# Performance work log

Hardware: AMD Instinct MI355X
Metric: run time of the kernel (lower is better)

The kernel has to match this reference:

```python
import jax, jax.numpy as jnp
import numpy as np


def _sample_plane(plane, coords):
    """torch.nn.functional.grid_sample, mode='bilinear', padding_mode='zeros',
    align_corners=True.  plane: [C,H,W]; coords: [N,2] with (x,y) in [-1,1]
    (x indexes W, y indexes H, as in torch grid convention).  Returns [N,C]."""
    C, H, W = plane.shape
    x = (coords[:, 0] + 1.0) * 0.5 * (W - 1)
    y = (coords[:, 1] + 1.0) * 0.5 * (H - 1)
    x0f = jnp.floor(x); y0f = jnp.floor(y)
    wx = x - x0f; wy = y - y0f

    def corner(yi, xi):
        valid = (xi >= 0) & (xi < W) & (yi >= 0) & (yi < H)
        xc = jnp.clip(xi, 0, W - 1).astype(jnp.int32)
        yc = jnp.clip(yi, 0, H - 1).astype(jnp.int32)
        return plane[:, yc, xc] * valid.astype(plane.dtype)  # [C,N]

    v00 = corner(y0f, x0f)
    v01 = corner(y0f, x0f + 1)
    v10 = corner(y0f + 1, x0f)
    v11 = corner(y0f + 1, x0f + 1)
    out = (v00 * (1 - wx) * (1 - wy) + v01 * wx * (1 - wy)
           + v10 * (1 - wx) * wy + v11 * wx * wy)
    return out.T  # [N,C]


_sample_batched = jax.vmap(_sample_plane)  # [B,C,H,W],[B,N,2] -> [B,N,C]


def setup_inputs() -> dict:
    key = jax.random.key(0)
    ks = jax.random.split(key, 8)
    B, N, C, R = 4, 131072, 32, 256
    triplanes = jax.random.normal(ks[0], (B, 3, C, R, R), jnp.float32) * 0.1
    coordinates = jax.random.uniform(ks[1], (B, N, 3), jnp.float32, -1.0, 1.0)
    # MLP weights ~ frequency_init(30) / first_layer_sine_init scales
    w0 = jax.random.uniform(ks[2], (128, C), jnp.float32, -1.0 / C, 1.0 / C)
    b0 = jnp.zeros((128,), jnp.float32)
    s1 = np.sqrt(6.0 / 128) / 30.0
    w1 = jax.random.uniform(ks[3], (128, 128), jnp.float32, -s1, s1)
    b1 = jnp.zeros((128,), jnp.float32)
    w2 = jax.random.uniform(ks[4], (1, 128), jnp.float32, -s1, s1)
    b2 = jnp.zeros((1,), jnp.float32)
    return {"triplanes": triplanes, "coordinates": coordinates,
            "w0": w0, "b0": b0, "w1": w1, "b1": b1, "w2": w2, "b2": b2}


def reference(triplanes, coordinates, w0, b0, w1, b1, w2, b2):
    # triplanes: [B,3,C,R,R]; coordinates: [B,N,3]
    xy = _sample_batched(triplanes[:, 0], coordinates[..., 0:2])   # (x,y)
    yz = _sample_batched(triplanes[:, 1], coordinates[..., 1:3])   # (y,z)
    xz = _sample_batched(triplanes[:, 2], coordinates[..., 0::2])  # (x,z)
    features = xy * yz * xz  # aggregate_fn == 'prod'; [B,N,C]
    h = jax.nn.relu(jnp.einsum('bnc,hc->bnh', features, w0) + b0)
    h = jax.nn.relu(jnp.einsum('bnh,gh->bng', h, w1) + b1)
    return jnp.einsum('bng,og->bno', h, w2) + b2  # [B,N,1]
```

## Files before the change

kernel.cpp:

```cpp
#include <hip/hip_runtime.h>
#include <hip/hip_bf16.h>
#include <cstddef>

#define RES 256
#define NCH 32
#define NPT 131072
#define NB  4

typedef _Float16 half8 __attribute__((ext_vector_type(8)));
typedef _Float16 half4 __attribute__((ext_vector_type(4)));
typedef float    f32x4 __attribute__((ext_vector_type(4)));

#define H0_STRIDE 136

__global__ __launch_bounds__(256) void transpose_fp16_kernel(
    const float* __restrict__ in, _Float16* __restrict__ out)
{
    __shared__ _Float16 tileh[NCH][2 * RES];
    const int bp = blockIdx.y;
    const int y2 = blockIdx.x;
    const int t  = threadIdx.x;

    const float4* src4 = (const float4*)(in + (size_t)bp * NCH * RES * RES);
    const int f4l = t & 127;
    const int chalf = t >> 7;
    #pragma unroll
    for (int i = 0; i < 16; ++i) {
        const int c = i * 2 + chalf;
        const float4 v = src4[(size_t)c * (RES * RES / 4) + y2 * 128 + f4l];
        half4 h = { (_Float16)v.x, (_Float16)v.y, (_Float16)v.z, (_Float16)v.w };
        *(half4*)&tileh[c][f4l * 4] = h;
    }
    __syncthreads();

    _Float16* dst = out + ((size_t)bp * RES * RES + (size_t)y2 * 512) * NCH;
    #pragma unroll
    for (int rep = 0; rep < 2; ++rep) {
        const int x = rep * 256 + t;
        #pragma unroll
        for (int cg = 0; cg < 4; ++cg) {
            half8 h;
            #pragma unroll
            for (int k = 0; k < 8; ++k)
                h[k] = tileh[cg * 8 + k][x];
            *(half8*)&dst[(size_t)x * NCH + cg * 8] = h;
        }
    }
}

__global__ __launch_bounds__(256) void prep_weights(
    const float* __restrict__ w0, const float* __restrict__ w1,
    _Float16* __restrict__ w0h, _Float16* __restrict__ w1h)
{
    const int i = blockIdx.x * 256 + threadIdx.x;
    if (i < 128 * NCH) w0h[i] = (_Float16)(w0[i] * 16.0f);
    if (i < 128 * 128) w1h[i] = (_Float16)w1[i];
}

__global__ __launch_bounds__(256, 4) void sample_kernel(
    const _Float16* __restrict__ planesT,
    const float* __restrict__ coords,
    _Float16* __restrict__ featOut)
{
    const int gid = blockIdx.x * 256 + threadIdx.x;
    const int pt  = gid >> 1;
    const int hf  = gid & 1;
    const int b   = pt >> 17;

    const float cx = coords[(size_t)pt * 3 + 0];
    const float cy = coords[(size_t)pt * 3 + 1];
    const float cz = coords[(size_t)pt * 3 + 2];

    float f[3][16];
    #pragma unroll
    for (int pl = 0; pl < 3; ++pl) {
        const float u = (pl == 0) ? cx : (pl == 1) ? cy : cx;
        const float v = (pl == 0) ? cy : cz;

        const float fx = (u + 1.0f) * 0.5f * (RES - 1);
        const float fy = (v + 1.0f) * 0.5f * (RES - 1);
        const float x0f = floorf(fx), y0f = floorf(fy);
        const float wx = fx - x0f, wy = fy - y0f;
        const int x0 = (int)x0f, y0 = (int)y0f;
        const bool vx1 = (x0 + 1) < RES;
        const bool vy1 = (y0 + 1) < RES;
        const int x1 = vx1 ? x0 + 1 : RES - 1;
        const int y1 = vy1 ? y0 + 1 : RES - 1;

        float w00 = (1.0f - wx) * (1.0f - wy);
        float w01 = wx * (1.0f - wy);
        float w10 = (1.0f - wx) * wy;
        float w11 = wx * wy;
        if (!vx1) { w01 = 0.0f; w11 = 0.0f; }
        if (!vy1) { w10 = 0.0f; w11 = 0.0f; }

        const _Float16* base = planesT
            + ((size_t)(b * 3 + pl) * RES * RES) * NCH + hf * 16;

        const half8* p00 = (const half8*)(base + (size_t)(y0 * RES + x0) * NCH);
        const half8* p01 = (const half8*)(base + (size_t)(y0 * RES + x1) * NCH);
        const half8* p10 = (const half8*)(base + (size_t)(y1 * RES + x0) * NCH);
        const half8* p11 = (const half8*)(base + (size_t)(y1 * RES + x1) * NCH);

        const half8 a00 = p00[0], b00 = p00[1];
        const half8 a01 = p01[0], b01 = p01[1];
        const half8 a10 = p10[0], b10 = p10[1];
        const half8 a11 = p11[0], b11 = p11[1];

        #pragma unroll
        for (int k = 0; k < 8; ++k) {
            f[pl][k] = fmaf((float)a11[k], w11, fmaf((float)a10[k], w10,
                       fmaf((float)a01[k], w01, (float)a00[k] * w00)));
            f[pl][8 + k] = fmaf((float)b11[k], w11, fmaf((float)b10[k], w10,
                           fmaf((float)b01[k], w01, (float)b00[k] * w00)));
        }
    }

    half8 o0, o1;
    #pragma unroll
    for (int k = 0; k < 8; ++k) {
        o0[k] = (_Float16)(f[0][k]     * f[1][k]     * f[2][k]     * 256.0f);
        o1[k] = (_Float16)(f[0][8 + k] * f[1][8 + k] * f[2][8 + k] * 256.0f);
    }
    _Float16* dst = featOut + (size_t)pt * NCH + hf * 16;
    *(half8*)&dst[0] = o0;
    *(half8*)&dst[8] = o1;
}

__global__ __launch_bounds__(256, 4) void gemm_kernel(
    const _Float16* __restrict__ feat,
    const _Float16* __restrict__ w0h,
    const _Float16* __restrict__ w1h,
    const float* __restrict__ b0, const float* __restrict__ b1,
    const float* __restrict__ w2, const float* __restrict__ b2,
    float* __restrict__ out)
{
    __shared__ __align__(16) _Float16 h0LDS[4][32 * H0_STRIDE];

    const int tid  = threadIdx.x;
    const int wv   = tid >> 6;
    const int lane = tid & 63;
    const int l15  = lane & 15;
    const int quad = lane >> 4;

    const int m0 = blockIdx.x * 128 + wv * 32;

    half8 a0[2];
    #pragma unroll
    for (int mt = 0; mt < 2; ++mt)
        a0[mt] = *(const half8*)&feat[(size_t)(m0 + mt * 16 + l15) * NCH + quad * 8];

    #pragma unroll 1
    for (int nt = 0; nt < 8; ++nt) {
        const half8 bfr = *(const half8*)&w0h[(nt * 16 + l15) * NCH + quad * 8];
        const float b0g = b0[nt * 16 + l15] * 4096.0f;
        f32x4 acc[2];
        #pragma unroll
        for (int mt = 0; mt < 2; ++mt) {
            acc[mt] = (f32x4){0.f, 0.f, 0.f, 0.f};
            acc[mt] = __builtin_amdgcn_mfma_f32_16x16x32_f16(
                a0[mt], bfr, acc[mt], 0, 0, 0);
        }
        #pragma unroll
        for (int mt = 0; mt < 2; ++mt)
            #pragma unroll
            for (int r = 0; r < 4; ++r) {
                const float hval = fmaxf(acc[mt][r] + b0g, 0.0f);
                h0LDS[wv][(mt * 16 + quad * 4 + r) * H0_STRIDE + nt * 16 + l15]
                    = (_Float16)hval;
            }
    }

    half8 a1[2][4];
    #pragma unroll
    for (int mt = 0; mt < 2; ++mt)
        #pragma unroll
        for (int ks = 0; ks < 4; ++ks)
            a1[mt][ks] = *(const half8*)
                &h0LDS[wv][(mt * 16 + l15) * H0_STRIDE + ks * 32 + quad * 8];

    float part[2][4];
    #pragma unroll
    for (int mt = 0; mt < 2; ++mt)
        #pragma unroll
        for (int r = 0; r < 4; ++r) part[mt][r] = 0.0f;

    #pragma unroll 1
    for (int nt = 0; nt < 8; ++nt) {
        const float b1g = b1[nt * 16 + l15] * 4096.0f;
        const float w2g = w2[nt * 16 + l15] * (1.0f / 4096.0f);
        f32x4 acc[2];
        #pragma unroll
        for (int mt = 0; mt < 2; ++mt) acc[mt] = (f32x4){0.f, 0.f, 0.f, 0.f};
        #pragma unroll
        for (int ks = 0; ks < 4; ++ks) {
            const half8 bfr = *(const half8*)
                &w1h[(nt * 16 + l15) * 128 + ks * 32 + quad * 8];
            #pragma unroll
            for (int mt = 0; mt < 2; ++mt)
                acc[mt] = __builtin_amdgcn_mfma_f32_16x16x32_f16(
                    a1[mt][ks], bfr, acc[mt], 0, 0, 0);
        }
        #pragma unroll
        for (int mt = 0; mt < 2; ++mt)
            #pragma unroll
            for (int r = 0; r < 4; ++r)
                part[mt][r] = fmaf(w2g, fmaxf(acc[mt][r] + b1g, 0.0f), part[mt][r]);
    }

    #pragma unroll
    for (int mt = 0; mt < 2; ++mt)
        #pragma unroll
        for (int r = 0; r < 4; ++r) {
            float s = part[mt][r];
            s += __shfl_xor(s, 1);
            s += __shfl_xor(s, 2);
            s += __shfl_xor(s, 4);
            s += __shfl_xor(s, 8);
            part[mt][r] = s;
        }

    if (l15 == 0) {
        const float bias2 = b2[0];
        #pragma unroll
        for (int mt = 0; mt < 2; ++mt)
            #pragma unroll
            for (int r = 0; r < 4; ++r)
                out[m0 + mt * 16 + quad * 4 + r] = part[mt][r] + bias2;
    }
}

__global__ __launch_bounds__(256) void fused_fallback(
    const float* __restrict__ planes, const float* __restrict__ coords,
    const float* __restrict__ w0, const float* __restrict__ b0,
    const float* __restrict__ w1, const float* __restrict__ b1,
    const float* __restrict__ w2, const float* __restrict__ b2,
    float* __restrict__ out)
{
    const int t = blockIdx.x * 256 + threadIdx.x;
    const int b = t >> 17;
    const float cx = coords[(size_t)t * 3 + 0];
    const float cy = coords[(size_t)t * 3 + 1];
    const float cz = coords[(size_t)t * 3 + 2];
    float feat[NCH];
    #pragma unroll
    for (int p = 0; p < 3; ++p) {
        const float u = (p == 0) ? cx : (p == 1) ? cy : cx;
        const float v = (p == 0) ? cy : cz;
        const float fx = (u + 1.0f) * 0.5f * (RES - 1);
        const float fy = (v + 1.0f) * 0.5f * (RES - 1);
        const float x0f = floorf(fx), y0f = floorf(fy);
        const float wx = fx - x0f, wy = fy - y0f;
        const int x0 = (int)x0f, y0 = (int)y0f;
        const bool vx1 = (x0 + 1) < RES, vy1 = (y0 + 1) < RES;
        const int x1 = vx1 ? x0 + 1 : RES - 1;
        const int y1 = vy1 ? y0 + 1 : RES - 1;
        float w00 = (1.0f - wx) * (1.0f - wy), w01 = wx * (1.0f - wy);
        float w10 = (1.0f - wx) * wy, w11 = wx * wy;
        if (!vx1) { w01 = 0.0f; w11 = 0.0f; }
        if (!vy1) { w10 = 0.0f; w11 = 0.0f; }
        const float* base = planes + (size_t)(b * 3 + p) * NCH * RES * RES;
        const float* p00 = base + (size_t)y0 * RES + x0;
        const float* p01 = base + (size_t)y0 * RES + x1;
        const float* p10 = base + (size_t)y1 * RES + x0;
        const float* p11 = base + (size_t)y1 * RES + x1;
        #pragma unroll
        for (int c = 0; c < NCH; ++c) {
            const size_t off = (size_t)c * RES * RES;
            float s = p00[off] * w00;
            s = fmaf(p01[off], w01, s);
            s = fmaf(p10[off], w10, s);
            s = fmaf(p11[off], w11, s);
            if (p == 0) feat[c] = s; else feat[c] *= s;
        }
    }
    float h0[128];
    #pragma unroll
    for (int g = 0; g < 128; ++g) {
        const float* wr = w0 + g * NCH;
        float aA = b0[g], aB = 0.0f;
        #pragma unroll
        for (int c = 0; c < NCH; c += 2) {
            aA = fmaf(wr[c], feat[c], aA);
            aB = fmaf(wr[c + 1], feat[c + 1], aB);
        }
        h0[g] = fmaxf(aA + aB, 0.0f);
    }
    float o = b2[0];
    for (int g = 0; g < 128; ++g) {
        const float* wr = w1 + g * 128;
        float aA = b1[g], aB = 0.0f, aC = 0.0f, aD = 0.0f;
        #pragma unroll
        for (int h = 0; h < 128; h += 4) {
            aA = fmaf(wr[h], h0[h], aA);
            aB = fmaf(wr[h + 1], h0[h + 1], aB);
            aC = fmaf(wr[h + 2], h0[h + 2], aC);
            aD = fmaf(wr[h + 3], h0[h + 3], aD);
        }
        o = fmaf(fmaxf((aA + aB) + (aC + aD), 0.0f), w2[g], o);
    }
    out[t] = o;
}

extern "C" void kernel_launch(void* const* d_in, const int* in_sizes, int n_in,
                              void* d_out, int out_size, void* d_ws, size_t ws_size,
                              hipStream_t stream)
{
    const float* trip   = (const float*)d_in[0];
    const float* coords = (const float*)d_in[1];
    const float* w0     = (const float*)d_in[2];
    const float* b0     = (const float*)d_in[3];
    const float* w1     = (const float*)d_in[4];
    const float* b1     = (const float*)d_in[5];
    const float* w2     = (const float*)d_in[6];
    const float* b2     = (const float*)d_in[7];
    float* out = (float*)d_out;

    const size_t planesTBytes = (size_t)NB * 3 * RES * RES * NCH * 2;
    const size_t w0hBytes  = 128 * NCH * 2;
    const size_t w1hBytes  = 128 * 128 * 2;
    const size_t featBytes = (size_t)NB * NPT * NCH * 2;
    const size_t needed = planesTBytes + w0hBytes + w1hBytes + featBytes;

    if (ws_size >= needed) {
        _Float16* planesT = (_Float16*)d_ws;
        _Float16* w0h     = (_Float16*)((char*)d_ws + planesTBytes);
        _Float16* w1h     = (_Float16*)((char*)d_ws + planesTBytes + w0hBytes);
        _Float16* featWS  = (_Float16*)((char*)d_ws + planesTBytes + w0hBytes + w1hBytes);

        transpose_fp16_kernel<<<dim3(RES / 2, NB * 3), 256, 0, stream>>>(trip, planesT);
        prep_weights<<<64, 256, 0, stream>>>(w0, w1, w0h, w1h);
        sample_kernel<<<(NB * NPT * 2) / 256, 256, 0, stream>>>(planesT, coords, featWS);
        gemm_kernel<<<(NB * NPT) / 128, 256, 0, stream>>>(
            featWS, w0h, w1h, b0, b1, w2, b2, out);
    } else {
        fused_fallback<<<(NB * NPT) / 256, 256, 0, stream>>>(
            trip, coords, w0, b0, w1, b1, w2, b2, out);
    }
}
```

Measured before the change: 333.4 us.

## Fuse triplane sampling into MLP kernel via shared-memory feature staging

Merges the sampling kernel and the MLP GEMM kernel into one. Each block now samples its 128 points into a padded LDS tile, which aliases the hidden-layer buffer, and then runs the MFMA layers directly on it. This removes the fp16 feature round-trip through global memory and one kernel launch. Bias and w2 values are preloaded into registers, and the transpose kernel now handles one row per block with a padded LDS tile. The trade-off is a lower occupancy hint (256,2), so fewer waves are resident to hide the gather latency.

```diff
diff --git a/kernel.cpp b/kernel.cpp
--- a/kernel.cpp
+++ b/kernel.cpp
@@ -11,40 +11,38 @@
 typedef _Float16 half4 __attribute__((ext_vector_type(4)));
 typedef float    f32x4 __attribute__((ext_vector_type(4)));
 
-#define H0_STRIDE 136
+#define FEAT_STRIDE 40
+#define H0_STRIDE   136
 
 __global__ __launch_bounds__(256) void transpose_fp16_kernel(
     const float* __restrict__ in, _Float16* __restrict__ out)
 {
-    __shared__ _Float16 tileh[NCH][2 * RES];
+    __shared__ _Float16 tileh[NCH][RES + 8];
     const int bp = blockIdx.y;
-    const int y2 = blockIdx.x;
+    const int y  = blockIdx.x;
     const int t  = threadIdx.x;
 
     const float4* src4 = (const float4*)(in + (size_t)bp * NCH * RES * RES);
-    const int f4l = t & 127;
-    const int chalf = t >> 7;
-    #pragma unroll
-    for (int i = 0; i < 16; ++i) {
-        const int c = i * 2 + chalf;
-        const float4 v = src4[(size_t)c * (RES * RES / 4) + y2 * 128 + f4l];
+    const int lane64 = t & 63;
+    const int cq     = t >> 6;
+    #pragma unroll
+    for (int i = 0; i < 8; ++i) {
+        const int c = cq * 8 + i;
+        const float4 v = src4[(size_t)c * (RES * RES / 4) + y * (RES / 4) + lane64];
         half4 h = { (_Float16)v.x, (_Float16)v.y, (_Float16)v.z, (_Float16)v.w };
-        *(half4*)&tileh[c][f4l * 4] = h;
+        *(half4*)&tileh[c][lane64 * 4] = h;
     }
     __syncthreads();
 
-    _Float16* dst = out + ((size_t)bp * RES * RES + (size_t)y2 * 512) * NCH;
-    #pragma unroll
-    for (int rep = 0; rep < 2; ++rep) {
-        const int x = rep * 256 + t;
-        #pragma unroll
-        for (int cg = 0; cg < 4; ++cg) {
-            half8 h;
-            #pragma unroll
-            for (int k = 0; k < 8; ++k)
-                h[k] = tileh[cg * 8 + k][x];
-            *(half8*)&dst[(size_t)x * NCH + cg * 8] = h;
-        }
+    _Float16* dst = out + ((size_t)bp * RES * RES + (size_t)y * RES) * NCH;
+    const int x = t;
+    #pragma unroll
+    for (int cg = 0; cg < 4; ++cg) {
+        half8 h;
+        #pragma unroll
+        for (int k = 0; k < 8; ++k)
+            h[k] = tileh[cg * 8 + k][x];
+        *(half8*)&dst[(size_t)x * NCH + cg * 8] = h;
     }
 }
 
@@ -57,85 +55,18 @@
     if (i < 128 * 128) w1h[i] = (_Float16)w1[i];
 }
 
-__global__ __launch_bounds__(256, 4) void sample_kernel(
+__global__ __launch_bounds__(256, 2) void fused_kernel(
     const _Float16* __restrict__ planesT,
     const float* __restrict__ coords,
-    _Float16* __restrict__ featOut)
-{
-    const int gid = blockIdx.x * 256 + threadIdx.x;
-    const int pt  = gid >> 1;
-    const int hf  = gid & 1;
-    const int b   = pt >> 17;
-
-    const float cx = coords[(size_t)pt * 3 + 0];
-    const float cy = coords[(size_t)pt * 3 + 1];
-    const float cz = coords[(size_t)pt * 3 + 2];
-
-    float f[3][16];
-    #pragma unroll
-    for (int pl = 0; pl < 3; ++pl) {
-        const float u = (pl == 0) ? cx : (pl == 1) ? cy : cx;
-        const float v = (pl == 0) ? cy : cz;
-
-        const float fx = (u + 1.0f) * 0.5f * (RES - 1);
-        const float fy = (v + 1.0f) * 0.5f * (RES - 1);
-        const float x0f = floorf(fx), y0f = floorf(fy);
-        const float wx = fx - x0f, wy = fy - y0f;
-        const int x0 = (int)x0f, y0 = (int)y0f;
-        const bool vx1 = (x0 + 1) < RES;
-        const bool vy1 = (y0 + 1) < RES;
-        const int x1 = vx1 ? x0 + 1 : RES - 1;
-        const int y1 = vy1 ? y0 + 1 : RES - 1;
-
-        float w00 = (1.0f - wx) * (1.0f - wy);
-        float w01 = wx * (1.0f - wy);
-        float w10 = (1.0f - wx) * wy;
-        float w11 = wx * wy;
-        if (!vx1) { w01 = 0.0f; w11 = 0.0f; }
-        if (!vy1) { w10 = 0.0f; w11 = 0.0f; }
-
-        const _Float16* base = planesT
-            + ((size_t)(b * 3 + pl) * RES * RES) * NCH + hf * 16;
-
-        const half8* p00 = (const half8*)(base + (size_t)(y0 * RES + x0) * NCH);
-        const half8* p01 = (const half8*)(base + (size_t)(y0 * RES + x1) * NCH);
-        const half8* p10 = (const half8*)(base + (size_t)(y1 * RES + x0) * NCH);
-        const half8* p11 = (const half8*)(base + (size_t)(y1 * RES + x1) * NCH);
-
-        const half8 a00 = p00[0], b00 = p00[1];
-        const half8 a01 = p01[0], b01 = p01[1];
-        const half8 a10 = p10[0], b10 = p10[1];
-        const half8 a11 = p11[0], b11 = p11[1];
-
-        #pragma unroll
-        for (int k = 0; k < 8; ++k) {
-            f[pl][k] = fmaf((float)a11[k], w11, fmaf((float)a10[k], w10,
-                       fmaf((float)a01[k], w01, (float)a00[k] * w00)));
-            f[pl][8 + k] = fmaf((float)b11[k], w11, fmaf((float)b10[k], w10,
-                           fmaf((float)b01[k], w01, (float)b00[k] * w00)));
-        }
-    }
-
-    half8 o0, o1;
-    #pragma unroll
-    for (int k = 0; k < 8; ++k) {
-        o0[k] = (_Float16)(f[0][k]     * f[1][k]     * f[2][k]     * 256.0f);
-        o1[k] = (_Float16)(f[0][8 + k] * f[1][8 + k] * f[2][8 + k] * 256.0f);
-    }
-    _Float16* dst = featOut + (size_t)pt * NCH + hf * 16;
-    *(half8*)&dst[0] = o0;
-    *(half8*)&dst[8] = o1;
-}
-
-__global__ __launch_bounds__(256, 4) void gemm_kernel(
-    const _Float16* __restrict__ feat,
     const _Float16* __restrict__ w0h,
     const _Float16* __restrict__ w1h,
     const float* __restrict__ b0, const float* __restrict__ b1,
     const float* __restrict__ w2, const float* __restrict__ b2,
     float* __restrict__ out)
 {
-    __shared__ __align__(16) _Float16 h0LDS[4][32 * H0_STRIDE];
+    __shared__ __align__(16) _Float16 smem[4 * 32 * H0_STRIDE];
+    _Float16* featLDS = smem;
+    _Float16* h0LDS   = smem;
 
     const int tid  = threadIdx.x;
     const int wv   = tid >> 6;
@@ -143,17 +74,91 @@
     const int l15  = lane & 15;
     const int quad = lane >> 4;
 
-    const int m0 = blockIdx.x * 128 + wv * 32;
+    {
+        const int p  = tid >> 1;
+        const int hf = tid & 1;
+        const int gp = blockIdx.x * 128 + p;
+        const int b  = gp >> 17;
+        const float cx = coords[(size_t)gp * 3 + 0];
+        const float cy = coords[(size_t)gp * 3 + 1];
+        const float cz = coords[(size_t)gp * 3 + 2];
+
+        float f[3][16];
+        #pragma unroll
+        for (int pl = 0; pl < 3; ++pl) {
+            const float u = (pl == 0) ? cx : (pl == 1) ? cy : cx;
+            const float v = (pl == 0) ? cy : cz;
+
+            const float fx = (u + 1.0f) * 0.5f * (RES - 1);
+            const float fy = (v + 1.0f) * 0.5f * (RES - 1);
+            const float x0f = floorf(fx), y0f = floorf(fy);
+            const float wx = fx - x0f, wy = fy - y0f;
+            const int x0 = (int)x0f, y0 = (int)y0f;
+            const bool vx1 = (x0 + 1) < RES;
+            const bool vy1 = (y0 + 1) < RES;
+            const int x1 = vx1 ? x0 + 1 : RES - 1;
+            const int y1 = vy1 ? y0 + 1 : RES - 1;
+
+            float w00 = (1.0f - wx) * (1.0f - wy);
+            float w01 = wx * (1.0f - wy);
+            float w10 = (1.0f - wx) * wy;
+            float w11 = wx * wy;
+            if (!vx1) { w01 = 0.0f; w11 = 0.0f; }
+            if (!vy1) { w10 = 0.0f; w11 = 0.0f; }
+
+            const _Float16* base = planesT
+                + ((size_t)(b * 3 + pl) * RES * RES) * NCH + hf * 16;
+
+            const half8* p00 = (const half8*)(base + (size_t)(y0 * RES + x0) * NCH);
+            const half8* p01 = (const half8*)(base + (size_t)(y0 * RES + x1) * NCH);
+            const half8* p10 = (const half8*)(base + (size_t)(y1 * RES + x0) * NCH);
+            const half8* p11 = (const half8*)(base + (size_t)(y1 * RES + x1) * NCH);
+
+            const half8 a00 = p00[0], b00 = p00[1];
+            const half8 a01 = p01[0], b01 = p01[1];
+            const half8 a10 = p10[0], b10 = p10[1];
+            const half8 a11 = p11[0], b11 = p11[1];
+
+            #pragma unroll
+            for (int k = 0; k < 8; ++k) {
+                f[pl][k] = fmaf((float)a11[k], w11, fmaf((float)a10[k], w10,
+                           fmaf((float)a01[k], w01, (float)a00[k] * w00)));
+                f[pl][8 + k] = fmaf((float)b11[k], w11, fmaf((float)b10[k], w10,
+                               fmaf((float)b01[k], w01, (float)b00[k] * w00)));
+            }
+        }
+        half8 o0, o1;
+        #pragma unroll
+        for (int k = 0; k < 8; ++k) {
+            o0[k] = (_Float16)(f[0][k]     * f[1][k]     * f[2][k]     * 256.0f);
+            o1[k] = (_Float16)(f[0][8 + k] * f[1][8 + k] * f[2][8 + k] * 256.0f);
+        }
+        *(half8*)&featLDS[p * FEAT_STRIDE + hf * 16 + 0] = o0;
+        *(half8*)&featLDS[p * FEAT_STRIDE + hf * 16 + 8] = o1;
+    }
+
+    const int m0l = wv * 32;
 
     half8 a0[2];
     #pragma unroll
     for (int mt = 0; mt < 2; ++mt)
-        a0[mt] = *(const half8*)&feat[(size_t)(m0 + mt * 16 + l15) * NCH + quad * 8];
+        a0[mt] = *(const half8*)&featLDS[(m0l + mt * 16 + l15) * FEAT_STRIDE + quad * 8];
+
+    __syncthreads();
+
+    float b0v[8], b1v[8], w2s[8];
+    #pragma unroll
+    for (int nt = 0; nt < 8; ++nt) {
+        b0v[nt] = b0[nt * 16 + l15] * 4096.0f;
+        b1v[nt] = b1[nt * 16 + l15] * 4096.0f;
+        w2s[nt] = w2[nt * 16 + l15] * (1.0f / 4096.0f);
+    }
+
+    _Float16* h0w = h0LDS + wv * 32 * H0_STRIDE;
 
     #pragma unroll 1
     for (int nt = 0; nt < 8; ++nt) {
         const half8 bfr = *(const half8*)&w0h[(nt * 16 + l15) * NCH + quad * 8];
-        const float b0g = b0[nt * 16 + l15] * 4096.0f;
         f32x4 acc[2];
         #pragma unroll
         for (int mt = 0; mt < 2; ++mt) {
@@ -165,8 +170,8 @@
         for (int mt = 0; mt < 2; ++mt)
             #pragma unroll
             for (int r = 0; r < 4; ++r) {
-                const float hval = fmaxf(acc[mt][r] + b0g, 0.0f);
-                h0LDS[wv][(mt * 16 + quad * 4 + r) * H0_STRIDE + nt * 16 + l15]
+                const float hval = fmaxf(acc[mt][r] + b0v[nt], 0.0f);
+                h0w[(mt * 16 + quad * 4 + r) * H0_STRIDE + nt * 16 + l15]
                     = (_Float16)hval;
             }
     }
@@ -177,7 +182,7 @@
         #pragma unroll
         for (int ks = 0; ks < 4; ++ks)
             a1[mt][ks] = *(const half8*)
-                &h0LDS[wv][(mt * 16 + l15) * H0_STRIDE + ks * 32 + quad * 8];
+                &h0w[(mt * 16 + l15) * H0_STRIDE + ks * 32 + quad * 8];
 
     float part[2][4];
     #pragma unroll
@@ -187,8 +192,6 @@
 
     #pragma unroll 1
     for (int nt = 0; nt < 8; ++nt) {
-        const float b1g = b1[nt * 16 + l15] * 4096.0f;
-        const float w2g = w2[nt * 16 + l15] * (1.0f / 4096.0f);
         f32x4 acc[2];
         #pragma unroll
         for (int mt = 0; mt < 2; ++mt) acc[mt] = (f32x4){0.f, 0.f, 0.f, 0.f};
@@ -205,7 +208,8 @@
         for (int mt = 0; mt < 2; ++mt)
             #pragma unroll
             for (int r = 0; r < 4; ++r)
-                part[mt][r] = fmaf(w2g, fmaxf(acc[mt][r] + b1g, 0.0f), part[mt][r]);
+                part[mt][r] = fmaf(w2s[nt], fmaxf(acc[mt][r] + b1v[nt], 0.0f),
+                                   part[mt][r]);
     }
 
     #pragma unroll
@@ -222,11 +226,12 @@
 
     if (l15 == 0) {
         const float bias2 = b2[0];
+        const int base = blockIdx.x * 128 + m0l;
         #pragma unroll
         for (int mt = 0; mt < 2; ++mt)
             #pragma unroll
             for (int r = 0; r < 4; ++r)
-                out[m0 + mt * 16 + quad * 4 + r] = part[mt][r] + bias2;
+                out[base + mt * 16 + quad * 4 + r] = part[mt][r] + bias2;
     }
 }
 
@@ -317,22 +322,19 @@
     float* out = (float*)d_out;
 
     const size_t planesTBytes = (size_t)NB * 3 * RES * RES * NCH * 2;
-    const size_t w0hBytes  = 128 * NCH * 2;
-    const size_t w1hBytes  = 128 * 128 * 2;
-    const size_t featBytes = (size_t)NB * NPT * NCH * 2;
-    const size_t needed = planesTBytes + w0hBytes + w1hBytes + featBytes;
+    const size_t w0hBytes = 128 * NCH * 2;
+    const size_t w1hBytes = 128 * 128 * 2;
+    const size_t needed = planesTBytes + w0hBytes + w1hBytes;
 
     if (ws_size >= needed) {
         _Float16* planesT = (_Float16*)d_ws;
         _Float16* w0h     = (_Float16*)((char*)d_ws + planesTBytes);
         _Float16* w1h     = (_Float16*)((char*)d_ws + planesTBytes + w0hBytes);
-        _Float16* featWS  = (_Float16*)((char*)d_ws + planesTBytes + w0hBytes + w1hBytes);
-
-        transpose_fp16_kernel<<<dim3(RES / 2, NB * 3), 256, 0, stream>>>(trip, planesT);
+
+        transpose_fp16_kernel<<<dim3(RES, NB * 3), 256, 0, stream>>>(trip, planesT);
         prep_weights<<<64, 256, 0, stream>>>(w0, w1, w0h, w1h);
-        sample_kernel<<<(NB * NPT * 2) / 256, 256, 0, stream>>>(planesT, coords, featWS);
-        gemm_kernel<<<(NB * NPT) / 128, 256, 0, stream>>>(
-            featWS, w0h, w1h, b0, b1, w2, b2, out);
+        fused_kernel<<<(NB * NPT) / 128, 256, 0, stream>>>(
+            planesT, coords, w0h, w1h, b0, b1, w2, b2, out);
     } else {
         fused_fallback<<<(NB * NPT) / 256, 256, 0, stream>>>(
             trip, coords, w0, b0, w1, b1, w2, b2, out);
```

Result: faster. 300.8 us (-9.8%).
